# Performance work log

Hardware: AMD Instinct MI355X
Metric: run time of the kernel (lower is better)

## Reference

```python
import jax, jax.numpy as jnp
import numpy as np

B, L, D, H, R = 2, 2048, 1024, 16, 512
HD = D // H  # head dim = 64
EPS = 1e-5


def layernorm(x, g, b):
    mu = jnp.mean(x, axis=-1, keepdims=True)
    var = jnp.mean(jnp.square(x - mu), axis=-1, keepdims=True)
    return (x - mu) * jax.lax.rsqrt(var + EPS) * g + b


def rel_pos_bias(res_pos, size):
    # Equivalent to the torch 'skew' causal_mask: bias[h, i, j] = res_pos[h, i-j]
    # if 0 <= i-j < R else -inf (causal + clipped relative distance).
    d = jnp.arange(size)[:, None] - jnp.arange(size)[None, :]  # (L, L)
    valid = (d >= 0) & (d < res_pos.shape[-1])
    gathered = res_pos[:, jnp.clip(d, 0, res_pos.shape[-1] - 1)]  # (H, L, L)
    return jnp.where(valid, gathered, -jnp.inf)


def setup_inputs() -> dict:
    key = jax.random.key(0)
    ks = jax.random.split(key, 12)
    s = lambda fan: 1.0 / np.sqrt(fan)
    return {
        "x": jax.random.normal(ks[0], (B, L, D), jnp.float32),
        "res_pos": jax.random.normal(ks[1], (H, R), jnp.float32) * 0.02,
        "w_qkv": jax.random.normal(ks[2], (D, 3 * D), jnp.float32) * s(D),
        "b_qkv": jnp.zeros((3 * D,), jnp.float32),
        "w_out": jax.random.normal(ks[3], (D, D), jnp.float32) * s(D),
        "b_out": jnp.zeros((D,), jnp.float32),
        "w1": jax.random.normal(ks[4], (D, 4 * D), jnp.float32) * s(D),
        "b1": jnp.zeros((4 * D,), jnp.float32),
        "w2": jax.random.normal(ks[5], (4 * D, D), jnp.float32) * s(4 * D),
        "b2": jnp.zeros((D,), jnp.float32),
        "ln1_g": jnp.ones((D,), jnp.float32),
        "ln1_b": jnp.zeros((D,), jnp.float32),
        "ln2_g": jnp.ones((D,), jnp.float32),
        "ln2_b": jnp.zeros((D,), jnp.float32),
    }


def reference(x, res_pos, w_qkv, b_qkv, w_out, b_out, w1, b1, w2, b2,
              ln1_g, ln1_b, ln2_g, ln2_b):
    b, l, _ = x.shape
    xn = layernorm(x, ln1_g, ln1_b)  # pre-norm
    qkv = xn @ w_qkv + b_qkv  # (B, L, 3D)
    q, k, v = jnp.split(qkv, 3, axis=-1)
    # (B, H, L, HD)
    q = q.reshape(b, l, H, HD).transpose(0, 2, 1, 3)
    k = k.reshape(b, l, H, HD).transpose(0, 2, 1, 3)
    v = v.reshape(b, l, H, HD).transpose(0, 2, 1, 3)
    scale = 1.0 / np.sqrt(HD)
    scores = jnp.einsum('bhqd,bhkd->bhqk', q, k) * scale
    scores = scores + rel_pos_bias(res_pos, l)[None]  # additive rel-pos causal mask
    attn = jax.nn.softmax(scores, axis=-1)
    ctx = jnp.einsum('bhqk,bhkd->bhqd', attn, v)
    ctx = ctx.transpose(0, 2, 1, 3).reshape(b, l, D)
    x = x + ctx @ w_out + b_out  # residual 1
    h = layernorm(x, ln2_g, ln2_b)
    h = jax.nn.relu(h @ w1 + b1) @ w2 + b2
    return x + h  # residual 2
```

## Files before the change

### kernel.cpp

```cpp
#include <hip/hip_runtime.h>
#include <math.h>

#define B_  2
#define L_  2048
#define D_  1024
#define H_  16
#define R_  512
#define HD_ 64
#define M_  (B_*L_)
#define EPS_ 1e-5f

typedef __attribute__((ext_vector_type(8))) short bf16x8;
typedef __attribute__((ext_vector_type(4))) float f32x4;

__device__ __forceinline__ unsigned short f2bf(float f) {
    unsigned int u = __float_as_uint(f);
    u += 0x7fffu + ((u >> 16) & 1u);
    return (unsigned short)(u >> 16);
}

__device__ __forceinline__ void gl2lds16(const void* g, void* l) {
    __builtin_amdgcn_global_load_lds(
        (const __attribute__((address_space(1))) unsigned int*)g,
        (__attribute__((address_space(3))) unsigned int*)l, 16, 0, 0);
}

__global__ __launch_bounds__(256) void ln_kernel(const float* __restrict__ x,
                                                 const float* __restrict__ g,
                                                 const float* __restrict__ b,
                                                 unsigned short* __restrict__ out) {
    int row = blockIdx.x;
    int t = threadIdx.x;
    const float4* xr = (const float4*)(x + (size_t)row * D_);
    float4 v = xr[t];
    float s  = v.x + v.y + v.z + v.w;
    float ss = v.x*v.x + v.y*v.y + v.z*v.z + v.w*v.w;
    #pragma unroll
    for (int o = 32; o > 0; o >>= 1) {
        s  += __shfl_down(s,  o);
        ss += __shfl_down(ss, o);
    }
    __shared__ float rs[4], rss[4];
    int wave = t >> 6, lane = t & 63;
    if (lane == 0) { rs[wave] = s; rss[wave] = ss; }
    __syncthreads();
    if (t == 0) {
        float a = 0.f, c = 0.f;
        for (int i = 0; i < 4; i++) { a += rs[i]; c += rss[i]; }
        rs[0] = a; rss[0] = c;
    }
    __syncthreads();
    float mean = rs[0] * (1.0f / D_);
    float var  = rss[0] * (1.0f / D_) - mean * mean;
    float inv  = rsqrtf(var + EPS_);
    float4 gv = ((const float4*)g)[t];
    float4 bv = ((const float4*)b)[t];
    ushort4 ob;
    ob.x = f2bf((v.x - mean) * inv * gv.x + bv.x);
    ob.y = f2bf((v.y - mean) * inv * gv.y + bv.y);
    ob.z = f2bf((v.z - mean) * inv * gv.z + bv.z);
    ob.w = f2bf((v.w - mean) * inv * gv.w + bv.w);
    ((ushort4*)(out + (size_t)row * D_))[t] = ob;
}

__global__ __launch_bounds__(256) void wtrans4_kernel(const float* __restrict__ w_qkv,
                                                      const float* __restrict__ w_out,
                                                      const float* __restrict__ w1,
                                                      const float* __restrict__ w2,
                                                      unsigned short* __restrict__ o_qkv,
                                                      unsigned short* __restrict__ o_out,
                                                      unsigned short* __restrict__ o_w1,
                                                      unsigned short* __restrict__ o_w2) {
    int id = blockIdx.x;
    const float* in; unsigned short* out; int K, N;
    if (id < 3072)      { in = w_qkv; out = o_qkv; K = 1024; N = 3072; }
    else if (id < 4096) { in = w_out; out = o_out; K = 1024; N = 1024; id -= 3072; }
    else if (id < 8192) { in = w1;    out = o_w1;  K = 1024; N = 4096; id -= 4096; }
    else                { in = w2;    out = o_w2;  K = 4096; N = 1024; id -= 8192; }
    int nb = N / 32;
    int bn = (id % nb) * 32, bk = (id / nb) * 32;

    __shared__ float tile[32][33];
    int t = threadIdx.x;
    int r = t >> 3, c4 = (t & 7) * 4;
    float4 v = *(const float4*)(in + (size_t)(bk + r) * N + bn + c4);
    tile[r][c4+0] = v.x; tile[r][c4+1] = v.y; tile[r][c4+2] = v.z; tile[r][c4+3] = v.w;
    __syncthreads();
    ushort4 o;
    o.x = f2bf(tile[c4+0][r]);
    o.y = f2bf(tile[c4+1][r]);
    o.z = f2bf(tile[c4+2][r]);
    o.w = f2bf(tile[c4+3][r]);
    *(ushort4*)(out + (size_t)(bn + r) * K + bk + c4) = o;
}

template<int BM, int KSPLIT, int RELU, int OUT_BF16>
__global__ __launch_bounds__(256) void gemm_mfma(const unsigned short* __restrict__ A,
                                                 const unsigned short* __restrict__ Wt,
                                                 const float* __restrict__ bias,
                                                 const float* __restrict__ res,
                                                 void* __restrict__ Cout,
                                                 int M, int N, int K) {
    constexpr int BN = 128;
    constexpr int BK = KSPLIT * 32;
    constexpr int TM = BM / 32;
    __shared__ __align__(16) unsigned short As[KSPLIT * BM * 32];
    __shared__ __align__(16) unsigned short Bs[KSPLIT * BN * 32];
    int t = threadIdx.x;
    int wave = t >> 6, lane = t & 63;
    int q = lane >> 4, cl = lane & 15;
    int bm = blockIdx.x * BM, bn = blockIdx.y * BN;
    int wm = (wave >> 1) * (BM / 2);
    int wn = (wave & 1) * 64;

    int sm = t >> 2;
    int sc = (t & 3) * 8;

    f32x4 acc[TM][4] = {};

    for (int kt = 0; kt < K; kt += BK) {
        __syncthreads();
        #pragma unroll
        for (int hh = 0; hh < KSPLIT; hh++) {
            #pragma unroll
            for (int s = 0; s < BM / 64; s++)
                gl2lds16(A + (size_t)(bm + s*64 + sm) * K + kt + hh*32 + sc,
                         &As[hh * BM * 32 + (s*64 + sm) * 32 + sc]);
            #pragma unroll
            for (int s = 0; s < 2; s++)
                gl2lds16(Wt + (size_t)(bn + s*64 + sm) * K + kt + hh*32 + sc,
                         &Bs[hh * BN * 32 + (s*64 + sm) * 32 + sc]);
        }
        __syncthreads();

        #pragma unroll
        for (int hh = 0; hh < KSPLIT; hh++) {
            bf16x8 af[TM], bfr[4];
            #pragma unroll
            for (int i = 0; i < TM; i++)
                af[i] = *(const bf16x8*)&As[hh * BM * 32 + (wm + i*16 + cl) * 32 + q*8];
            #pragma unroll
            for (int j = 0; j < 4; j++)
                bfr[j] = *(const bf16x8*)&Bs[hh * BN * 32 + (wn + j*16 + cl) * 32 + q*8];
            #pragma unroll
            for (int i = 0; i < TM; i++)
                #pragma unroll
                for (int j = 0; j < 4; j++)
                    acc[i][j] = __builtin_amdgcn_mfma_f32_16x16x32_bf16(
                                    af[i], bfr[j], acc[i][j], 0, 0, 0);
        }
    }

    #pragma unroll
    for (int i = 0; i < TM; i++) {
        #pragma unroll
        for (int j = 0; j < 4; j++) {
            #pragma unroll
            for (int r = 0; r < 4; r++) {
                int row = bm + wm + i*16 + q*4 + r;
                int col = bn + wn + j*16 + cl;
                float v = acc[i][j][r] + bias[col];
                if (RELU) v = fmaxf(v, 0.0f);
                if (res)  v += res[(size_t)row * N + col];
                if (OUT_BF16)
                    ((unsigned short*)Cout)[(size_t)row * N + col] = f2bf(v);
                else
                    ((float*)Cout)[(size_t)row * N + col] = v;
            }
        }
    }
}

#define AP_ 80
__global__ __launch_bounds__(256) void attn_mfma_kernel(const unsigned short* __restrict__ qkv,
                                                        const float* __restrict__ res_pos,
                                                        unsigned short* __restrict__ ctx) {
    int q0 = blockIdx.x * 64;
    int h  = blockIdx.y;
    int b  = blockIdx.z;
    int t  = threadIdx.x;
    int w  = t >> 6, lane = t & 63;
    int quad = lane >> 4, cl = lane & 15;

    __shared__ __align__(16) unsigned short sQP[64 * AP_];
    __shared__ __align__(16) unsigned short sK [64 * AP_];
    __shared__ __align__(16) unsigned short sVt[64 * AP_];
    __shared__ float sBias[R_];

    const int bL = b * L_;
    const unsigned short* base = qkv + (size_t)bL * 3072;

    #pragma unroll
    for (int c = t; c < 512; c += 256) {
        int row = c >> 3, off = (c & 7) * 8;
        uint4 v = *(const uint4*)(base + (size_t)(q0 + row) * 3072 + h * HD_ + off);
        *(uint4*)&sQP[row * AP_ + off] = v;
    }
    sBias[t]       = res_pos[h * R_ + t]       - 20.0f;
    sBias[t + 256] = res_pos[h * R_ + t + 256] - 20.0f;
    __syncthreads();

    bf16x8 qf0 = *(const bf16x8*)&sQP[(w*16 + cl) * AP_ + quad*8];
    bf16x8 qf1 = *(const bf16x8*)&sQP[(w*16 + cl) * AP_ + 32 + quad*8];

    f32x4 accO[4] = {};
    float l_r[4] = {0.f, 0.f, 0.f, 0.f};

    int klo = q0 - (R_ - 1); if (klo < 0) klo = 0;
    int kt0 = klo & ~63;
    const float scale = 0.125f;

    for (int k0 = kt0; k0 <= q0; k0 += 64) {
        __syncthreads();
        #pragma unroll
        for (int c = t; c < 512; c += 256) {
            int row = c >> 3, off = (c & 7) * 8;
            uint4 v = *(const uint4*)(base + (size_t)(k0 + row) * 3072 + D_ + h * HD_ + off);
            *(uint4*)&sK[row * AP_ + off] = v;
        }
        {
            int c2 = t & 31, dg = t >> 5;
            int cl_ = c2 & 15, jb = (c2 >> 4) * 2;
            int ka = jb * 16 + cl_;
            const unsigned short* va = base + (size_t)(k0 + ka) * 3072 + 2*D_ + h * HD_ + dg*8;
            uint4 a4 = *(const uint4*)va;
            uint4 b4 = *(const uint4*)(va + (size_t)16 * 3072);
            const unsigned short* pa = (const unsigned short*)&a4;
            const unsigned short* pb = (const unsigned short*)&b4;
            #pragma unroll
            for (int i = 0; i < 8; i++) {
                unsigned int packed = (unsigned int)pa[i] | ((unsigned int)pb[i] << 16);
                *(unsigned int*)&sVt[(dg*8 + i) * AP_ + 4*cl_ + jb] = packed;
            }
        }
        __syncthreads();

        f32x4 sacc[4] = {};
        #pragma unroll
        for (int j = 0; j < 4; j++) {
            bf16x8 kf0 = *(const bf16x8*)&sK[(j*16 + cl) * AP_ + quad*8];
            bf16x8 kf1 = *(const bf16x8*)&sK[(j*16 + cl) * AP_ + 32 + quad*8];
            sacc[j] = __builtin_amdgcn_mfma_f32_16x16x32_bf16(qf0, kf0, sacc[j], 0, 0, 0);
            sacc[j] = __builtin_amdgcn_mfma_f32_16x16x32_bf16(qf1, kf1, sacc[j], 0, 0, 0);
        }

        #pragma unroll
        for (int r = 0; r < 4; r++) {
            int qrow = q0 + w*16 + quad*4 + r;
            unsigned short pk[4];
            float lacc = 0.f;
            #pragma unroll
            for (int j = 0; j < 4; j++) {
                int key = k0 + j*16 + cl;
                int diff = qrow - key;
                bool valid = ((unsigned)diff) < (unsigned)R_;
                int dc = valid ? diff : 0;
                float p = valid ? __expf(fmaf(sacc[j][r], scale, sBias[dc])) : 0.f;
                lacc += p;
                pk[j] = f2bf(p);
            }
            l_r[r] += lacc;
            unsigned int lo = (unsigned int)pk[0] | ((unsigned int)pk[1] << 16);
            unsigned int hi = (unsigned int)pk[2] | ((unsigned int)pk[3] << 16);
            uint2 pv; pv.x = lo; pv.y = hi;
            *(uint2*)&sQP[(w*16 + quad*4 + r) * AP_ + 4*cl] = pv;
        }
        __syncthreads();

        bf16x8 pf0 = *(const bf16x8*)&sQP[(w*16 + cl) * AP_ + quad*8];
        bf16x8 pf1 = *(const bf16x8*)&sQP[(w*16 + cl) * AP_ + 32 + quad*8];
        #pragma unroll
        for (int j = 0; j < 4; j++) {
            bf16x8 vf0 = *(const bf16x8*)&sVt[(j*16 + cl) * AP_ + quad*8];
            bf16x8 vf1 = *(const bf16x8*)&sVt[(j*16 + cl) * AP_ + 32 + quad*8];
            accO[j] = __builtin_amdgcn_mfma_f32_16x16x32_bf16(pf0, vf0, accO[j], 0, 0, 0);
            accO[j] = __builtin_amdgcn_mfma_f32_16x16x32_bf16(pf1, vf1, accO[j], 0, 0, 0);
        }
    }

    #pragma unroll
    for (int r = 0; r < 4; r++) {
        float l = l_r[r];
        #pragma unroll
        for (int o = 8; o > 0; o >>= 1) l += __shfl_xor(l, o);
        float inv = 1.0f / l;
        int row = bL + q0 + w*16 + quad*4 + r;
        #pragma unroll
        for (int j = 0; j < 4; j++)
            ctx[(size_t)row * D_ + h * HD_ + j*16 + cl] = f2bf(accO[j][r] * inv);
    }
}

extern "C" void kernel_launch(void* const* d_in, const int* in_sizes, int n_in,
                              void* d_out, int out_size, void* d_ws, size_t ws_size,
                              hipStream_t stream) {
    const float* x      = (const float*)d_in[0];
    const float* res_pos= (const float*)d_in[1];
    const float* w_qkv  = (const float*)d_in[2];
    const float* b_qkv  = (const float*)d_in[3];
    const float* w_out  = (const float*)d_in[4];
    const float* b_out  = (const float*)d_in[5];
    const float* w1     = (const float*)d_in[6];
    const float* b1     = (const float*)d_in[7];
    const float* w2     = (const float*)d_in[8];
    const float* b2     = (const float*)d_in[9];
    const float* ln1_g  = (const float*)d_in[10];
    const float* ln1_b  = (const float*)d_in[11];
    const float* ln2_g  = (const float*)d_in[12];
    const float* ln2_b  = (const float*)d_in[13];
    float* out = (float*)d_out;
    char* ws = (char*)d_ws;

    unsigned short* act_bf = (unsigned short*)ws;
    unsigned short* wqkvT  = (unsigned short*)(ws + ((size_t)8  << 20));
    unsigned short* woutT  = (unsigned short*)(ws + ((size_t)14 << 20));
    unsigned short* w1T    = (unsigned short*)(ws + ((size_t)16 << 20));
    unsigned short* w2T    = (unsigned short*)(ws + ((size_t)24 << 20));
    unsigned short* qkv_bf = (unsigned short*)(ws + ((size_t)32 << 20));
    unsigned short* h1_bf  = (unsigned short*)(ws + ((size_t)32 << 20));

    wtrans4_kernel<<<12288, 256, 0, stream>>>(w_qkv, w_out, w1, w2,
                                              wqkvT, woutT, w1T, w2T);
    ln_kernel<<<M_, 256, 0, stream>>>(x, ln1_g, ln1_b, act_bf);
    gemm_mfma<128,1,0,1><<<dim3(M_/128, 3072/128), 256, 0, stream>>>(
        act_bf, wqkvT, b_qkv, nullptr, qkv_bf, M_, 3072, 1024);
    attn_mfma_kernel<<<dim3(L_/64, H_, B_), 256, 0, stream>>>(qkv_bf, res_pos, act_bf);
    gemm_mfma<64,1,0,0><<<dim3(M_/64, 1024/128), 256, 0, stream>>>(
        act_bf, woutT, b_out, x, out, M_, 1024, 1024);
    ln_kernel<<<M_, 256, 0, stream>>>(out, ln2_g, ln2_b, act_bf);
    gemm_mfma<128,1,1,1><<<dim3(M_/128, 4096/128), 256, 0, stream>>>(
        act_bf, w1T, b1, nullptr, h1_bf, M_, 4096, 1024);
    gemm_mfma<64,2,0,0><<<dim3(M_/64, 1024/128), 256, 0, stream>>>(
        h1_bf, w2T, b2, out, out, M_, 1024, 4096);
}
```

Measured before the change: 355.3 us.

## Swizzle GEMM LDS layout, fuse weight prep with LN1, retune GEMM tiles

Applies an XOR swizzle to the global-to-LDS source column and the matching fragment read offset in the MFMA GEMM, so LDS fragment reads spread across banks instead of conflicting. The weight transpose/convert kernel and the first layernorm are merged into one launch so the two launches become one. The QKV, out-proj and FFN1 GEMMs switch to 64-row tiles with a 64-wide K step, giving more blocks and fewer barriers per K. Smaller M tiles reduce B-tile reuse and add global traffic.

```diff
diff --git a/kernel.cpp b/kernel.cpp
--- a/kernel.cpp
+++ b/kernel.cpp
@@ -23,6 +23,77 @@
     __builtin_amdgcn_global_load_lds(
         (const __attribute__((address_space(1))) unsigned int*)g,
         (__attribute__((address_space(3))) unsigned int*)l, 16, 0, 0);
+}
+
+__global__ __launch_bounds__(256) void prep_kernel(const float* __restrict__ w_qkv,
+                                                   const float* __restrict__ w_out,
+                                                   const float* __restrict__ w1,
+                                                   const float* __restrict__ w2,
+                                                   const float* __restrict__ x,
+                                                   const float* __restrict__ ln1_g,
+                                                   const float* __restrict__ ln1_b,
+                                                   unsigned short* __restrict__ o_qkv,
+                                                   unsigned short* __restrict__ o_out,
+                                                   unsigned short* __restrict__ o_w1,
+                                                   unsigned short* __restrict__ o_w2,
+                                                   unsigned short* __restrict__ xn) {
+    int id = blockIdx.x;
+    int t = threadIdx.x;
+
+    if (id >= 12288) {
+        int row = id - 12288;
+        const float4* xr = (const float4*)(x + (size_t)row * D_);
+        float4 v = xr[t];
+        float s  = v.x + v.y + v.z + v.w;
+        float ss = v.x*v.x + v.y*v.y + v.z*v.z + v.w*v.w;
+        #pragma unroll
+        for (int o = 32; o > 0; o >>= 1) {
+            s  += __shfl_down(s,  o);
+            ss += __shfl_down(ss, o);
+        }
+        __shared__ float rs[4], rss[4];
+        int wave = t >> 6, lane = t & 63;
+        if (lane == 0) { rs[wave] = s; rss[wave] = ss; }
+        __syncthreads();
+        if (t == 0) {
+            float a = 0.f, c = 0.f;
+            for (int i = 0; i < 4; i++) { a += rs[i]; c += rss[i]; }
+            rs[0] = a; rss[0] = c;
+        }
+        __syncthreads();
+        float mean = rs[0] * (1.0f / D_);
+        float var  = rss[0] * (1.0f / D_) - mean * mean;
+        float inv  = rsqrtf(var + EPS_);
+        float4 gv = ((const float4*)ln1_g)[t];
+        float4 bv = ((const float4*)ln1_b)[t];
+        ushort4 ob;
+        ob.x = f2bf((v.x - mean) * inv * gv.x + bv.x);
+        ob.y = f2bf((v.y - mean) * inv * gv.y + bv.y);
+        ob.z = f2bf((v.z - mean) * inv * gv.z + bv.z);
+        ob.w = f2bf((v.w - mean) * inv * gv.w + bv.w);
+        ((ushort4*)(xn + (size_t)row * D_))[t] = ob;
+        return;
+    }
+
+    const float* in; unsigned short* out; int K, N;
+    if (id < 3072)      { in = w_qkv; out = o_qkv; K = 1024; N = 3072; }
+    else if (id < 4096) { in = w_out; out = o_out; K = 1024; N = 1024; id -= 3072; }
+    else if (id < 8192) { in = w1;    out = o_w1;  K = 1024; N = 4096; id -= 4096; }
+    else                { in = w2;    out = o_w2;  K = 4096; N = 1024; id -= 8192; }
+    int nb = N / 32;
+    int bn = (id % nb) * 32, bk = (id / nb) * 32;
+
+    __shared__ float tile[32][33];
+    int r = t >> 3, c4 = (t & 7) * 4;
+    float4 v = *(const float4*)(in + (size_t)(bk + r) * N + bn + c4);
+    tile[r][c4+0] = v.x; tile[r][c4+1] = v.y; tile[r][c4+2] = v.z; tile[r][c4+3] = v.w;
+    __syncthreads();
+    ushort4 o;
+    o.x = f2bf(tile[c4+0][r]);
+    o.y = f2bf(tile[c4+1][r]);
+    o.z = f2bf(tile[c4+2][r]);
+    o.w = f2bf(tile[c4+3][r]);
+    *(ushort4*)(out + (size_t)(bn + r) * K + bk + c4) = o;
 }
 
 __global__ __launch_bounds__(256) void ln_kernel(const float* __restrict__ x,
@@ -61,37 +132,6 @@
     ob.z = f2bf((v.z - mean) * inv * gv.z + bv.z);
     ob.w = f2bf((v.w - mean) * inv * gv.w + bv.w);
     ((ushort4*)(out + (size_t)row * D_))[t] = ob;
-}
-
-__global__ __launch_bounds__(256) void wtrans4_kernel(const float* __restrict__ w_qkv,
-                                                      const float* __restrict__ w_out,
-                                                      const float* __restrict__ w1,
-                                                      const float* __restrict__ w2,
-                                                      unsigned short* __restrict__ o_qkv,
-                                                      unsigned short* __restrict__ o_out,
-                                                      unsigned short* __restrict__ o_w1,
-                                                      unsigned short* __restrict__ o_w2) {
-    int id = blockIdx.x;
-    const float* in; unsigned short* out; int K, N;
-    if (id < 3072)      { in = w_qkv; out = o_qkv; K = 1024; N = 3072; }
-    else if (id < 4096) { in = w_out; out = o_out; K = 1024; N = 1024; id -= 3072; }
-    else if (id < 8192) { in = w1;    out = o_w1;  K = 1024; N = 4096; id -= 4096; }
-    else                { in = w2;    out = o_w2;  K = 4096; N = 1024; id -= 8192; }
-    int nb = N / 32;
-    int bn = (id % nb) * 32, bk = (id / nb) * 32;
-
-    __shared__ float tile[32][33];
-    int t = threadIdx.x;
-    int r = t >> 3, c4 = (t & 7) * 4;
-    float4 v = *(const float4*)(in + (size_t)(bk + r) * N + bn + c4);
-    tile[r][c4+0] = v.x; tile[r][c4+1] = v.y; tile[r][c4+2] = v.z; tile[r][c4+3] = v.w;
-    __syncthreads();
-    ushort4 o;
-    o.x = f2bf(tile[c4+0][r]);
-    o.y = f2bf(tile[c4+1][r]);
-    o.z = f2bf(tile[c4+2][r]);
-    o.w = f2bf(tile[c4+3][r]);
-    *(ushort4*)(out + (size_t)(bn + r) * K + bk + c4) = o;
 }
 
 template<int BM, int KSPLIT, int RELU, int OUT_BF16>
@@ -113,8 +153,12 @@
     int wm = (wave >> 1) * (BM / 2);
     int wn = (wave & 1) * 64;
 
-    int sm = t >> 2;
-    int sc = (t & 3) * 8;
+    int sm  = t >> 2;
+    int scx = t & 3;
+    int ssrc = (scx ^ (sm & 3)) * 8;
+    int sdst = scx * 8;
+
+    int qa = (q ^ (cl & 3)) * 8;
 
     f32x4 acc[TM][4] = {};
 
@@ -124,12 +168,12 @@
         for (int hh = 0; hh < KSPLIT; hh++) {
             #pragma unroll
             for (int s = 0; s < BM / 64; s++)
-                gl2lds16(A + (size_t)(bm + s*64 + sm) * K + kt + hh*32 + sc,
-                         &As[hh * BM * 32 + (s*64 + sm) * 32 + sc]);
+                gl2lds16(A + (size_t)(bm + s*64 + sm) * K + kt + hh*32 + ssrc,
+                         &As[hh * BM * 32 + (s*64 + sm) * 32 + sdst]);
             #pragma unroll
             for (int s = 0; s < 2; s++)
-                gl2lds16(Wt + (size_t)(bn + s*64 + sm) * K + kt + hh*32 + sc,
-                         &Bs[hh * BN * 32 + (s*64 + sm) * 32 + sc]);
+                gl2lds16(Wt + (size_t)(bn + s*64 + sm) * K + kt + hh*32 + ssrc,
+                         &Bs[hh * BN * 32 + (s*64 + sm) * 32 + sdst]);
         }
         __syncthreads();
 
@@ -138,10 +182,10 @@
             bf16x8 af[TM], bfr[4];
             #pragma unroll
             for (int i = 0; i < TM; i++)
-                af[i] = *(const bf16x8*)&As[hh * BM * 32 + (wm + i*16 + cl) * 32 + q*8];
+                af[i] = *(const bf16x8*)&As[hh * BM * 32 + (wm + i*16 + cl) * 32 + qa];
             #pragma unroll
             for (int j = 0; j < 4; j++)
-                bfr[j] = *(const bf16x8*)&Bs[hh * BN * 32 + (wn + j*16 + cl) * 32 + q*8];
+                bfr[j] = *(const bf16x8*)&Bs[hh * BN * 32 + (wn + j*16 + cl) * 32 + qa];
             #pragma unroll
             for (int i = 0; i < TM; i++)
                 #pragma unroll
@@ -319,16 +363,16 @@
     unsigned short* qkv_bf = (unsigned short*)(ws + ((size_t)32 << 20));
     unsigned short* h1_bf  = (unsigned short*)(ws + ((size_t)32 << 20));
 
-    wtrans4_kernel<<<12288, 256, 0, stream>>>(w_qkv, w_out, w1, w2,
-                                              wqkvT, woutT, w1T, w2T);
-    ln_kernel<<<M_, 256, 0, stream>>>(x, ln1_g, ln1_b, act_bf);
-    gemm_mfma<128,1,0,1><<<dim3(M_/128, 3072/128), 256, 0, stream>>>(
+    prep_kernel<<<16384, 256, 0, stream>>>(w_qkv, w_out, w1, w2,
+                                           x, ln1_g, ln1_b,
+                                           wqkvT, woutT, w1T, w2T, act_bf);
+    gemm_mfma<64,2,0,1><<<dim3(M_/64, 3072/128), 256, 0, stream>>>(
         act_bf, wqkvT, b_qkv, nullptr, qkv_bf, M_, 3072, 1024);
     attn_mfma_kernel<<<dim3(L_/64, H_, B_), 256, 0, stream>>>(qkv_bf, res_pos, act_bf);
-    gemm_mfma<64,1,0,0><<<dim3(M_/64, 1024/128), 256, 0, stream>>>(
+    gemm_mfma<64,2,0,0><<<dim3(M_/64, 1024/128), 256, 0, stream>>>(
         act_bf, woutT, b_out, x, out, M_, 1024, 1024);
     ln_kernel<<<M_, 256, 0, stream>>>(out, ln2_g, ln2_b, act_bf);
-    gemm_mfma<128,1,1,1><<<dim3(M_/128, 4096/128), 256, 0, stream>>>(
+    gemm_mfma<64,2,1,1><<<dim3(M_/64, 4096/128), 256, 0, stream>>>(
         act_bf, w1T, b1, nullptr, h1_bf, M_, 4096, 1024);
     gemm_mfma<64,2,0,0><<<dim3(M_/64, 1024/128), 256, 0, stream>>>(
         h1_bf, w2T, b2, out, out, M_, 1024, 4096);
```

After: 349.4 us. Within noise of the previous version (-1.7%).
